# Kernel optimization log

Hardware: AMD Instinct MI355X
Metric: run time of the kernel (lower is better)

Reference implementation:

```python
import jax, jax.numpy as jnp
import numpy as np

NG = 1024      # graphs
NPG = 128      # nodes per graph (forced by lin1 = Linear(128*hid, 128))
N = NG * NPG   # 131072 nodes
DEG = 16       # avg in-graph degree
E = N * DEG    # 2,097,152 edges
IN, H = 4, 64


def setup_inputs() -> dict:
    key = jax.random.key(0)
    ks = jax.random.split(key, 24)
    x = jax.random.normal(ks[0], (N, IN), jnp.float32)
    # edges constrained within each 128-node graph
    src = jax.random.randint(ks[1], (E,), 0, NPG)
    dst = jax.random.randint(ks[2], (E,), 0, NPG)
    off = jnp.repeat(jnp.arange(NG, dtype=jnp.int32) * NPG, NPG * DEG)
    edge_index = jnp.stack([src.astype(jnp.int32) + off, dst.astype(jnp.int32) + off])
    g = lambda k, shp, fan: jax.random.normal(k, shp, jnp.float32) / np.float32(np.sqrt(fan))
    return {
        "x": x, "edge_index": edge_index,
        # GATv2Conv(4->64)
        "Wl": g(ks[3], (IN, H), IN), "bl": jnp.zeros((H,), jnp.float32),
        "Wr": g(ks[4], (IN, H), IN), "br": jnp.zeros((H,), jnp.float32),
        "att_v2": g(ks[5], (H,), H), "b_v2": jnp.zeros((H,), jnp.float32),
        # GATConv #1 (64->64)
        "Wg1": g(ks[6], (H, H), H), "as1": g(ks[7], (H,), H),
        "ad1": g(ks[8], (H,), H), "bg1": jnp.zeros((H,), jnp.float32),
        # GATConv #2 (64->64)
        "Wg2": g(ks[9], (H, H), H), "as2": g(ks[10], (H,), H),
        "ad2": g(ks[11], (H,), H), "bg2": jnp.zeros((H,), jnp.float32),
        # LayerNorm(64)
        "ln_g": jnp.ones((H,), jnp.float32), "ln_b": jnp.zeros((H,), jnp.float32),
        # heads: Linear(128*64 -> 128), Linear(128 -> 1)
        "W1": g(ks[12], (NPG * H, 128), NPG * H), "b1": jnp.zeros((128,), jnp.float32),
        "W2": g(ks[13], (128, 1), 128), "b2": jnp.zeros((1,), jnp.float32),
    }


def _seg_softmax(logits, seg):
    # stable softmax over edges grouped by destination node
    m = jax.ops.segment_max(logits, seg, num_segments=N)
    ex = jnp.exp(logits - m[seg])
    s = jax.ops.segment_sum(ex, seg, num_segments=N)
    return ex / (s[seg] + 1e-16)


def _gatv2(x, src, dst, Wl, bl, Wr, br, att, bias):
    xl = x @ Wl + bl                       # source transform [N,H]
    xr = x @ Wr + br                       # target transform [N,H]
    e = jax.nn.leaky_relu(xl[src] + xr[dst], 0.2) @ att   # [E]
    a = _seg_softmax(e, dst)
    out = jax.ops.segment_sum(a[:, None] * xl[src], dst, num_segments=N)
    return out + bias


def _gat(x, src, dst, W, a_src, a_dst, bias):
    # GATConv default: add self-loops
    loop = jnp.arange(N, dtype=src.dtype)
    s2 = jnp.concatenate([src, loop]); d2 = jnp.concatenate([dst, loop])
    xw = x @ W                             # [N,H]
    al_s = xw @ a_src; al_d = xw @ a_dst   # per-node attention halves [N]
    e = jax.nn.leaky_relu(al_s[s2] + al_d[d2], 0.2)
    a = _seg_softmax(e, d2)
    out = jax.ops.segment_sum(a[:, None] * xw[s2], d2, num_segments=N)
    return out + bias


def _layernorm(x, g, b, eps=1e-5):
    mu = jnp.mean(x, -1, keepdims=True)
    var = jnp.mean(jnp.square(x - mu), -1, keepdims=True)
    return (x - mu) * jax.lax.rsqrt(var + eps) * g + b


def reference(x, edge_index, Wl, bl, Wr, br, att_v2, b_v2,
              Wg1, as1, ad1, bg1, Wg2, as2, ad2, bg2,
              ln_g, ln_b, W1, b1, W2, b2):
    src, dst = edge_index[0], edge_index[1]
    h = jax.nn.leaky_relu(_gatv2(x, src, dst, Wl, bl, Wr, br, att_v2, b_v2), 0.01)
    h = _layernorm(h, ln_g, ln_b)
    h = jax.nn.relu(_gat(h, src, dst, Wg1, as1, ad1, bg1))
    h = jax.nn.relu(_gat(h, src, dst, Wg2, as2, ad2, bg2))
    # linearize: batch is sorted with exactly NPG nodes per graph -> reshape
    h = h.reshape(NG, NPG * H)
    h = jax.nn.leaky_relu(h @ W1 + b1, 0.01)
    return jax.nn.sigmoid(h @ W2 + b2)     # [NG, 1]
```

## Files before the change

### kernel.cpp

```cpp
#include <hip/hip_runtime.h>
#include <hip/hip_bf16.h>
#include <hip/hip_fp16.h>

#define NGRAPH 1024
#define NPG 128
#define EPG 2048
#define ETOT (NGRAPH*NPG*16)

typedef unsigned int uint;
typedef unsigned short ushort_t;
typedef __attribute__((ext_vector_type(2))) _Float16 h2v;
typedef __attribute__((ext_vector_type(8))) _Float16 h8v;
typedef __attribute__((ext_vector_type(4))) float f32x4;

#define MFMA16H __builtin_amdgcn_mfma_f32_16x16x32_f16
#define FDOT2(a,b,c) __builtin_amdgcn_fdot2((a),(b),(c),false)

union U1H2 { uint u; h2v h; };
union U4H8 { uint4 u; h8v h; };
union U4H2 { uint4 u; h2v h[4]; };

__device__ __forceinline__ float lrelu(float x, float s){ return fmaxf(x, x*s); }
__device__ __forceinline__ uint pkh(float a, float b){
  U1H2 t; t.h.x = (_Float16)a; t.h.y = (_Float16)b; return t.u;
}
__device__ __forceinline__ ushort_t hfb(float v){
  union { _Float16 h; ushort_t u; } t; t.h = (_Float16)v; return t.u;
}
__device__ __forceinline__ float2 uph(uint u){
  U1H2 t; t.u = u;
  return float2{(float)t.h.x, (float)t.h.y};
}
#define DPP_ADD(v, ctrl) ((v) + __int_as_float(__builtin_amdgcn_update_dpp(0, __float_as_int(v), (ctrl), 0xF, 0xF, false)))

__device__ __forceinline__ int oswz(int r, int p){ return (r<<5) | ((((p>>2) ^ (r & 7))<<2) | (p & 3)); }
__device__ __forceinline__ int obase(int r, int oc){ return (r<<5) | (((oc) ^ (r & 7))<<2); }

__device__ __forceinline__ void fma8(float* acc, uint4 q, float a){
  float2 f0 = uph(q.x), f1 = uph(q.y), f2 = uph(q.z), f3 = uph(q.w);
  acc[0] += a*f0.x; acc[1] += a*f0.y;
  acc[2] += a*f1.x; acc[3] += a*f1.y;
  acc[4] += a*f2.x; acc[5] += a*f2.y;
  acc[6] += a*f3.x; acc[7] += a*f3.y;
}

__device__ __forceinline__ float dotp(uint ul, uint ur, h2v a2, float acc){
  U1H2 l, r; l.u = ul; r.u = ur;
  h2v v = l.h + r.h;
  U1H2 sv; sv.h = v;
  U1H2 av; av.u = sv.u & 0x7FFF7FFFu;
  h2v c6; c6.x = (_Float16)0.6f; c6.y = (_Float16)0.6f;
  h2v c4; c4.x = (_Float16)0.4f; c4.y = (_Float16)0.4f;
  h2v w = v * c6 + av.h * c4;
  return FDOT2(w, a2, acc);
}

#define O_A   0
#define O_B   4096
#define O_EVA 8192
#define O_ED  10240
#define O_WS  11264
#define O_SOF 11392
#define O_ALS 11457
#define O_ALD 11585
#define SM_SZ 11713

__global__ __launch_bounds__(256, 3) void gnn_fused(
    const float* __restrict__ x, const int* __restrict__ ei,
    const float* __restrict__ Wl, const float* __restrict__ bl,
    const float* __restrict__ Wr, const float* __restrict__ br,
    const float* __restrict__ att, const float* __restrict__ bv2,
    const float* __restrict__ Wg1, const float* __restrict__ as1,
    const float* __restrict__ ad1, const float* __restrict__ bg1,
    const float* __restrict__ Wg2, const float* __restrict__ as2,
    const float* __restrict__ ad2, const float* __restrict__ bg2,
    const float* __restrict__ lng, const float* __restrict__ lnb,
    uint* __restrict__ hout)
{
  __shared__ uint SM[SM_SZ];
  float*    eva    = (float*)(SM + O_EVA);
  ushort_t* edsL   = (ushort_t*)(SM + O_ED);
  ushort_t* soff16 = (ushort_t*)(SM + O_SOF);
  float*    als    = (float*)(SM + O_ALS);
  float*    ald    = (float*)(SM + O_ALD);
  float*    was    = (float*)(SM + O_WS);
  float*    wad    = was + 64;
  ushort_t* wgA16  = (ushort_t*)(SM + O_A);
  ushort_t* wg16   = (ushort_t*)(SM + O_EVA);

  const int g    = blockIdx.x;
  const int tid  = threadIdx.x;
  const int lane = tid & 63;
  const int wv   = tid >> 6;
  const int lw   = lane & 15;
  const int lq   = lane >> 4;
  const int sl   = lane & 7;
  const int grp  = lane >> 3;
  const int ebase = g * EPG;

  {
    int* spos = (int*)(SM + O_EVA);
    if (tid < NPG) spos[tid] = 0;
    __syncthreads();
    for (int e = tid; e < EPG; e += 256)
      atomicAdd(&spos[ei[ETOT + ebase + e] - g*NPG], 1);
    __syncthreads();
    if (wv == 0) {
      int c0 = spos[lane], c1 = spos[lane + 64];
      #pragma unroll
      for (int o = 1; o < 64; o <<= 1) { int t = __shfl_up(c0, o); if (lane >= o) c0 += t; }
      #pragma unroll
      for (int o = 1; o < 64; o <<= 1) { int t = __shfl_up(c1, o); if (lane >= o) c1 += t; }
      int tot0 = __shfl(c0, 63);
      soff16[lane + 1]  = (ushort_t)c0;
      soff16[lane + 65] = (ushort_t)(c1 + tot0);
      if (lane == 0) soff16[0] = 0;
    }
    __syncthreads();
    if (tid < NPG) spos[tid] = soff16[tid];
    __syncthreads();
    for (int e = tid; e < EPG; e += 256) {
      int s = ei[ebase + e] - g*NPG;
      int d = ei[ETOT + ebase + e] - g*NPG;
      int p = atomicAdd(&spos[d], 1);
      edsL[p] = (ushort_t)(s | (d << 8));
    }
  }

  {
    const int pl = lane & 31, hb = lane >> 5;
    const float2 wl0 = *(const float2*)&Wl[0*64 + 2*pl];
    const float2 wl1 = *(const float2*)&Wl[1*64 + 2*pl];
    const float2 wl2 = *(const float2*)&Wl[2*64 + 2*pl];
    const float2 wl3 = *(const float2*)&Wl[3*64 + 2*pl];
    const float2 wr0 = *(const float2*)&Wr[0*64 + 2*pl];
    const float2 wr1 = *(const float2*)&Wr[1*64 + 2*pl];
    const float2 wr2 = *(const float2*)&Wr[2*64 + 2*pl];
    const float2 wr3 = *(const float2*)&Wr[3*64 + 2*pl];
    const float2 blp = *(const float2*)&bl[2*pl];
    const float2 brp = *(const float2*)&br[2*pl];
    const float4* x4 = (const float4*)x + (size_t)g * NPG;
    for (int st = 0; st < 16; st++) {
      int i = st*8 + wv*2 + hb;
      float4 xi = x4[i];
      float l0 = blp.x + xi.x*wl0.x + xi.y*wl1.x + xi.z*wl2.x + xi.w*wl3.x;
      float l1 = blp.y + xi.x*wl0.y + xi.y*wl1.y + xi.z*wl2.y + xi.w*wl3.y;
      float r0 = brp.x + xi.x*wr0.x + xi.y*wr1.x + xi.z*wr2.x + xi.w*wr3.x;
      float r1 = brp.y + xi.x*wr0.y + xi.y*wr1.y + xi.z*wr2.y + xi.w*wr3.y;
      SM[O_A + oswz(i, pl)] = pkh(l0, l1);
      SM[O_B + oswz(i, pl)] = pkh(r0, r1);
    }
  }
  __syncthreads();

  {
    h2v att2[32];
    #pragma unroll
    for (int p2 = 0; p2 < 32; p2++) {
      att2[p2].x = (_Float16)att[2*p2];
      att2[p2].y = (_Float16)att[2*p2 + 1];
    }
    for (int it = 0; it < 8; it++) {
      int e  = tid + it*256;
      int sd = edsL[e];
      int s  = sd & 127, d = sd >> 8;
      float acc = 0.f;
      #pragma unroll
      for (int c = 0; c < 8; c++) {
        uint4 ql = *(uint4*)&SM[O_A + obase(s, c)];
        uint4 qr = *(uint4*)&SM[O_B + obase(d, c)];
        acc = dotp(ql.x, qr.x, att2[4*c+0], acc);
        acc = dotp(ql.y, qr.y, att2[4*c+1], acc);
        acc = dotp(ql.z, qr.z, att2[4*c+2], acc);
        acc = dotp(ql.w, qr.w, att2[4*c+3], acc);
      }
      eva[e] = acc;
    }
  }
  __syncthreads();

  {
    const int dd = tid >> 4, sl16 = tid & 15;
    for (int it = 0; it < 8; it++) {
      int d = it*16 + dd;
      int p0 = soff16[d], p1 = soff16[d+1];
      float m = -1e30f;
      for (int p = p0 + sl16; p < p1; p += 16) m = fmaxf(m, eva[p]);
      #pragma unroll
      for (int o = 1; o < 16; o <<= 1) m = fmaxf(m, __shfl_xor(m, o));
      float ss = 0.f;
      for (int p = p0 + sl16; p < p1; p += 16) {
        float ex = __expf(eva[p] - m); ss += ex; eva[p] = ex;
      }
      #pragma unroll
      for (int o = 1; o < 16; o <<= 1) ss += __shfl_xor(ss, o);
      if (sl16 == 0) als[d] = 1.f / (ss + 1e-16f);
    }
  }
  __syncthreads();

  {
    float2 bvA = *(const float2*)&bv2[sl*8];
    float2 bvB = *(const float2*)&bv2[sl*8 + 2];
    float2 bvC = *(const float2*)&bv2[sl*8 + 4];
    float2 bvD = *(const float2*)&bv2[sl*8 + 6];
    for (int pass = 0; pass < 4; pass++) {
      int d  = wv*32 + pass*8 + grp;
      int p0 = soff16[d], p1 = soff16[d+1];
      float acc[8] = {0,0,0,0,0,0,0,0};
      if (p0 < p1) {
        int sN = edsL[p0] & 127;
        uint4 qN = *(uint4*)&SM[O_A + obase(sN, sl)];
        float wN = eva[p0];
        for (int e = p0; e < p1; e++) {
          uint4 ql = qN; float w = wN;
          if (e + 1 < p1) {
            sN = edsL[e+1] & 127;
            qN = *(uint4*)&SM[O_A + obase(sN, sl)];
            wN = eva[e+1];
          }
          fma8(acc, ql, w);
        }
      }
      float nm = als[d];
      uint4 o;
      o.x = pkh(lrelu(acc[0]*nm+bvA.x,0.01f), lrelu(acc[1]*nm+bvA.y,0.01f));
      o.y = pkh(lrelu(acc[2]*nm+bvB.x,0.01f), lrelu(acc[3]*nm+bvB.y,0.01f));
      o.z = pkh(lrelu(acc[4]*nm+bvC.x,0.01f), lrelu(acc[5]*nm+bvC.y,0.01f));
      o.w = pkh(lrelu(acc[6]*nm+bvD.x,0.01f), lrelu(acc[7]*nm+bvD.y,0.01f));
      *(uint4*)&SM[O_B + obase(d, sl)] = o;
    }
  }
  __syncthreads();

  {
    int pl = lane & 31, hb = lane >> 5;
    float2 gv = *(const float2*)&lng[2*pl];
    float2 bv = *(const float2*)&lnb[2*pl];
    h2v one2; one2.x = (_Float16)1.f; one2.y = (_Float16)1.f;
    for (int it = 0; it < 16; it++) {
      int d = it*8 + wv*2 + hb;
      uint w = SM[O_B + oswz(d, pl)];
      U1H2 t; t.u = w;
      float s1 = FDOT2(t.h, one2, 0.f);
      float s2 = FDOT2(t.h, t.h, 0.f);
      #pragma unroll
      for (int o = 1; o < 32; o <<= 1) { s1 += __shfl_xor(s1, o); s2 += __shfl_xor(s2, o); }
      float mu  = s1 * 0.015625f;
      float var = s2 * 0.015625f - mu*mu;
      float rs  = rsqrtf(var + 1e-5f);
      float2 f = uph(w);
      SM[O_B + oswz(d, pl)] = pkh((f.x-mu)*rs*gv.x + bv.x, (f.y-mu)*rs*gv.y + bv.y);
    }
  }
  __syncthreads();

  for (int layer = 0; layer < 2; layer++) {
    const float* Wg  = layer ? Wg2 : Wg1;
    const float* avs = layer ? as2 : as1;
    const float* avd = layer ? ad2 : ad1;
    const float* bg  = layer ? bg2 : bg1;

    if (tid < 128) {
      const float* av = (tid < 64) ? avs : avd;
      float* dst = (tid < 64) ? was : wad;
      int k = tid & 63;
      float acc = 0.f;
      #pragma unroll
      for (int jj = 0; jj < 16; jj++) {
        float4 w = *(const float4*)&Wg[k*64 + jj*4];
        float4 a = *(const float4*)&av[jj*4];
        acc += w.x*a.x + w.y*a.y + w.z*a.z + w.w*a.w;
      }
      dst[k] = acc;
    } else {
      int t2 = tid - 128;
      #pragma unroll
      for (int i = 0; i < 8; i++) {
        int idx = t2 + i*128;
        int k = idx >> 4, j4 = (idx & 15)*4;
        float4 w = *(const float4*)&Wg[k*64 + j4];
        wg16[oswz(j4+0, k>>1)*2 + (k&1)] = hfb(w.x);
        wg16[oswz(j4+1, k>>1)*2 + (k&1)] = hfb(w.y);
        wg16[oswz(j4+2, k>>1)*2 + (k&1)] = hfb(w.z);
        wg16[oswz(j4+3, k>>1)*2 + (k&1)] = hfb(w.w);
      }
    }
    __syncthreads();

    {
      U4H8 a0t, a1t;
      a0t.u = *(uint4*)&SM[O_EVA + obase(16*wv + lw, lq)];
      a1t.u = *(uint4*)&SM[O_EVA + obase(16*wv + lw, 4+lq)];
      int j0 = 16*wv + lq*4;
      #pragma unroll
      for (int nt = 0; nt < 8; nt++) {
        int d = nt*16 + lw;
        U4H8 b0t, b1t;
        b0t.u = *(uint4*)&SM[O_B + obase(d, lq)];
        b1t.u = *(uint4*)&SM[O_B + obase(d, 4+lq)];
        f32x4 c = {0.f,0.f,0.f,0.f};
        c = MFMA16H(a0t.h, b0t.h, c, 0, 0, 0);
        c = MFMA16H(a1t.h, b1t.h, c, 0, 0, 0);
        #pragma unroll
        for (int rg = 0; rg < 4; rg++) {
          int j = j0 + rg;
          wgA16[oswz(d, j>>1)*2 + (j&1)] = hfb(c[rg]);
        }
      }
      h2v ws2[4], wd2[4];
      #pragma unroll
      for (int q2 = 0; q2 < 4; q2++) {
        float2 a = *(float2*)&was[sl*8 + 2*q2];
        float2 b = *(float2*)&wad[sl*8 + 2*q2];
        ws2[q2].x = (_Float16)a.x; ws2[q2].y = (_Float16)a.y;
        wd2[q2].x = (_Float16)b.x; wd2[q2].y = (_Float16)b.y;
      }
      for (int ps = 0; ps < 4; ps++) {
        int n = ps*32 + (tid >> 3);
        U4H2 q; q.u = *(uint4*)&SM[O_B + obase(n, sl)];
        float sa = 0.f, sd = 0.f;
        #pragma unroll
        for (int q2 = 0; q2 < 4; q2++) {
          sa = FDOT2(q.h[q2], ws2[q2], sa);
          sd = FDOT2(q.h[q2], wd2[q2], sd);
        }
        sa = DPP_ADD(sa, 0x111); sa = DPP_ADD(sa, 0x112); sa = DPP_ADD(sa, 0x114);
        sd = DPP_ADD(sd, 0x111); sd = DPP_ADD(sd, 0x112); sd = DPP_ADD(sd, 0x114);
        if ((lane & 7) == 7) { als[n] = sa; ald[n] = sd; }
      }
    }
    __syncthreads();

    for (int it = 0; it < 8; it++) {
      int e  = tid + it*256;
      int sd = edsL[e];
      eva[e] = lrelu(als[sd & 127] + ald[sd >> 8], 0.2f);
    }
    __syncthreads();

    {
      const int dd = tid >> 4, sl16 = tid & 15;
      for (int it = 0; it < 8; it++) {
        int d = it*16 + dd;
        int p0 = soff16[d], p1 = soff16[d+1];
        float lgs = lrelu(als[d] + ald[d], 0.2f);
        float m = lgs;
        for (int p = p0 + sl16; p < p1; p += 16) m = fmaxf(m, eva[p]);
        #pragma unroll
        for (int o = 1; o < 16; o <<= 1) m = fmaxf(m, __shfl_xor(m, o));
        float ex0 = __expf(lgs - m);
        float ss = 0.f;
        for (int p = p0 + sl16; p < p1; p += 16) {
          float ex = __expf(eva[p] - m); ss += ex; eva[p] = ex;
        }
        #pragma unroll
        for (int o = 1; o < 16; o <<= 1) ss += __shfl_xor(ss, o);
        if (sl16 == 0) {
          als[d] = ex0;
          ald[d] = 1.f / (ss + ex0 + 1e-16f);
        }
      }
    }
    __syncthreads();

    {
      float2 bgA = *(const float2*)&bg[sl*8];
      float2 bgB = *(const float2*)&bg[sl*8 + 2];
      float2 bgC = *(const float2*)&bg[sl*8 + 4];
      float2 bgD = *(const float2*)&bg[sl*8 + 6];
      for (int pass = 0; pass < 4; pass++) {
        int d  = wv*32 + pass*8 + grp;
        int p0 = soff16[d], p1 = soff16[d+1];
        float acc[8] = {0,0,0,0,0,0,0,0};
        fma8(acc, *(uint4*)&SM[O_A + obase(d, sl)], als[d]);
        if (p0 < p1) {
          int sN = edsL[p0] & 127;
          uint4 qN = *(uint4*)&SM[O_A + obase(sN, sl)];
          float wN = eva[p0];
          for (int e = p0; e < p1; e++) {
            uint4 ql = qN; float w = wN;
            if (e + 1 < p1) {
              sN = edsL[e+1] & 127;
              qN = *(uint4*)&SM[O_A + obase(sN, sl)];
              wN = eva[e+1];
            }
            fma8(acc, ql, w);
          }
        }
        float nm = ald[d];
        uint4 o;
        o.x = pkh(fmaxf(acc[0]*nm+bgA.x,0.f), fmaxf(acc[1]*nm+bgA.y,0.f));
        o.y = pkh(fmaxf(acc[2]*nm+bgB.x,0.f), fmaxf(acc[3]*nm+bgB.y,0.f));
        o.z = pkh(fmaxf(acc[4]*nm+bgC.x,0.f), fmaxf(acc[5]*nm+bgC.y,0.f));
        o.w = pkh(fmaxf(acc[6]*nm+bgD.x,0.f), fmaxf(acc[7]*nm+bgD.y,0.f));
        *(uint4*)&SM[O_B + obase(d, sl)] = o;
      }
    }
    __syncthreads();
  }

  {
    uint* hg = hout + (size_t)g * 4096;
    #pragma unroll
    for (int i = 0; i < 16; i++) {
      int idx = tid + i*256;
      hg[idx] = SM[O_B + oswz(idx >> 5, idx & 31)];
    }
  }
}

__global__ __launch_bounds__(256) void head_gemm(
    const uint* __restrict__ hbuf, const float* __restrict__ W1,
    float* __restrict__ partial)
{
  __shared__ uint sAh[2048];
  __shared__ uint sBh[4096];
  const int tid = threadIdx.x, lane = tid & 63, wv = tid >> 6;
  const int lw = lane & 15, lq = lane >> 4;
  const int g0 = blockIdx.x * 64;
  const int ks = blockIdx.y;
  f32x4 acc[8];
  #pragma unroll
  for (int i = 0; i < 8; i++) acc[i] = f32x4{0.f,0.f,0.f,0.f};

  for (int ch = 0; ch < 8; ch++) {
    int pb  = ks*256 + ch*32;
    int kk0 = ks*512 + ch*64;
    #pragma unroll
    for (int i = 0; i < 2; i++) {
      int idx = tid + i*256; int r = idx >> 3, q4 = idx & 7;
      uint4 v = *(const uint4*)&hbuf[(size_t)(g0+r)*4096 + pb + q4*4];
      *(uint4*)&sAh[(r<<5) | ((q4 ^ (r & 7))<<2)] = v;
    }
    #pragma unroll
    for (int i = 0; i < 16; i++) {
      int idx = tid + i*256;
      int c = idx & 127, kp = idx >> 7;
      int kk = kk0 + 2*kp;
      sBh[oswz(c, kp)] = pkh(W1[(size_t)kk*128 + c], W1[(size_t)(kk+1)*128 + c]);
    }
    __syncthreads();
    U4H8 a0t, a1t;
    a0t.u = *(uint4*)&sAh[obase(16*wv + lw, lq)];
    a1t.u = *(uint4*)&sAh[obase(16*wv + lw, 4+lq)];
    #pragma unroll
    for (int nt = 0; nt < 8; nt++) {
      int c = nt*16 + lw;
      U4H8 b0t, b1t;
      b0t.u = *(uint4*)&sBh[obase(c, lq)];
      b1t.u = *(uint4*)&sBh[obase(c, 4+lq)];
      acc[nt] = MFMA16H(a0t.h, b0t.h, acc[nt], 0, 0, 0);
      acc[nt] = MFMA16H(a1t.h, b1t.h, acc[nt], 0, 0, 0);
    }
    __syncthreads();
  }
  float* pp = partial + (size_t)ks*131072;
  #pragma unroll
  for (int nt = 0; nt < 8; nt++) {
    int c = nt*16 + lw;
    int r0 = g0 + 16*wv + lq*4;
    #pragma unroll
    for (int rg = 0; rg < 4; rg++)
      pp[(size_t)(r0+rg)*128 + c] = acc[nt][rg];
  }
}

__global__ __launch_bounds__(256) void head_out(
    const float* __restrict__ partial, const float* __restrict__ b1,
    const float* __restrict__ W2, const float* __restrict__ b2,
    float* __restrict__ out)
{
  const int tid = threadIdx.x;
  const int gl  = tid >> 5;
  const int c4  = tid & 31;
  const int g   = blockIdx.x*8 + gl;
  float4 v = *(const float4*)&b1[c4*4];
  #pragma unroll
  for (int s = 0; s < 16; s++) {
    float4 p = *(const float4*)&partial[(size_t)s*131072 + (size_t)g*128 + c4*4];
    v.x += p.x; v.y += p.y; v.z += p.z; v.w += p.w;
  }
  float4 w = *(const float4*)&W2[c4*4];
  float t = lrelu(v.x,0.01f)*w.x + lrelu(v.y,0.01f)*w.y
          + lrelu(v.z,0.01f)*w.z + lrelu(v.w,0.01f)*w.w;
  #pragma unroll
  for (int m = 1; m < 32; m <<= 1) t += __shfl_xor(t, m);
  if (c4 == 0) out[g] = 1.f / (1.f + __expf(-(t + b2[0])));
}

extern "C" void kernel_launch(void* const* d_in, const int* in_sizes, int n_in,
                              void* d_out, int out_size, void* d_ws, size_t ws_size,
                              hipStream_t stream) {
  const float* x   = (const float*)d_in[0];
  const int*   ei  = (const int*)  d_in[1];
  const float* Wl  = (const float*)d_in[2];
  const float* bl_ = (const float*)d_in[3];
  const float* Wr  = (const float*)d_in[4];
  const float* br_ = (const float*)d_in[5];
  const float* att = (const float*)d_in[6];
  const float* bv2 = (const float*)d_in[7];
  const float* Wg1 = (const float*)d_in[8];
  const float* as1 = (const float*)d_in[9];
  const float* ad1 = (const float*)d_in[10];
  const float* bg1 = (const float*)d_in[11];
  const float* Wg2 = (const float*)d_in[12];
  const float* as2 = (const float*)d_in[13];
  const float* ad2 = (const float*)d_in[14];
  const float* bg2 = (const float*)d_in[15];
  const float* lng = (const float*)d_in[16];
  const float* lnb = (const float*)d_in[17];
  const float* W1  = (const float*)d_in[18];
  const float* b1  = (const float*)d_in[19];
  const float* W2  = (const float*)d_in[20];
  const float* b2  = (const float*)d_in[21];
  float* out = (float*)d_out;

  uint*  hbuf    = (uint*)d_ws;
  float* partial = (float*)((char*)d_ws + (size_t)16*1024*1024);

  gnn_fused<<<NGRAPH, 256, 0, stream>>>(x, ei, Wl, bl_, Wr, br_, att, bv2,
      Wg1, as1, ad1, bg1, Wg2, as2, ad2, bg2, lng, lnb, hbuf);
  head_gemm<<<dim3(16, 16), 256, 0, stream>>>(hbuf, W1, partial);
  head_out<<<128, 256, 0, stream>>>(partial, b1, W2, b2, out);
}
```

Baseline: 310.2 us.

## Factor GATv2 logits into per-node terms, fp16 aggregation, deeper head split-K

```diff
diff --git a/kernel.cpp b/kernel.cpp
--- a/kernel.cpp
+++ b/kernel.cpp
@@ -42,17 +42,6 @@
   acc[2] += a*f1.x; acc[3] += a*f1.y;
   acc[4] += a*f2.x; acc[5] += a*f2.y;
   acc[6] += a*f3.x; acc[7] += a*f3.y;
-}
-
-__device__ __forceinline__ float dotp(uint ul, uint ur, h2v a2, float acc){
-  U1H2 l, r; l.u = ul; r.u = ur;
-  h2v v = l.h + r.h;
-  U1H2 sv; sv.h = v;
-  U1H2 av; av.u = sv.u & 0x7FFF7FFFu;
-  h2v c6; c6.x = (_Float16)0.6f; c6.y = (_Float16)0.6f;
-  h2v c4; c4.x = (_Float16)0.4f; c4.y = (_Float16)0.4f;
-  h2v w = v * c6 + av.h * c4;
-  return FDOT2(w, a2, acc);
 }
 
 #define O_A   0
@@ -153,28 +142,46 @@
   }
   __syncthreads();
 
-  {
-    h2v att2[32];
+  h2v a06[4], a04[4];
+  #pragma unroll
+  for (int q2 = 0; q2 < 4; q2++) {
+    float2 a = *(const float2*)&att[sl*8 + 2*q2];
+    a06[q2].x = (_Float16)(0.6f*a.x); a06[q2].y = (_Float16)(0.6f*a.y);
+    a04[q2].x = (_Float16)(0.4f*a.x); a04[q2].y = (_Float16)(0.4f*a.y);
+  }
+
+  for (int ps = 0; ps < 4; ps++) {
+    int n = ps*32 + (tid >> 3);
+    U4H2 ql; ql.u = *(uint4*)&SM[O_A + obase(n, sl)];
+    U4H2 qr; qr.u = *(uint4*)&SM[O_B + obase(n, sl)];
+    float su = 0.f, sw = 0.f;
     #pragma unroll
-    for (int p2 = 0; p2 < 32; p2++) {
-      att2[p2].x = (_Float16)att[2*p2];
-      att2[p2].y = (_Float16)att[2*p2 + 1];
-    }
-    for (int it = 0; it < 8; it++) {
-      int e  = tid + it*256;
+    for (int q2 = 0; q2 < 4; q2++) {
+      su = FDOT2(ql.h[q2], a06[q2], su);
+      sw = FDOT2(qr.h[q2], a06[q2], sw);
+    }
+    su = DPP_ADD(su, 0x111); su = DPP_ADD(su, 0x112); su = DPP_ADD(su, 0x114);
+    sw = DPP_ADD(sw, 0x111); sw = DPP_ADD(sw, 0x112); sw = DPP_ADD(sw, 0x114);
+    if ((lane & 7) == 7) { als[n] = su; ald[n] = sw; }
+  }
+  __syncthreads();
+
+  {
+    for (int step = 0; step < 64; step++) {
+      int e  = wv*512 + step*8 + grp;
       int sd = edsL[e];
       int s  = sd & 127, d = sd >> 8;
+      U4H2 ql; ql.u = *(uint4*)&SM[O_A + obase(s, sl)];
+      U4H2 qr; qr.u = *(uint4*)&SM[O_B + obase(d, sl)];
       float acc = 0.f;
       #pragma unroll
-      for (int c = 0; c < 8; c++) {
-        uint4 ql = *(uint4*)&SM[O_A + obase(s, c)];
-        uint4 qr = *(uint4*)&SM[O_B + obase(d, c)];
-        acc = dotp(ql.x, qr.x, att2[4*c+0], acc);
-        acc = dotp(ql.y, qr.y, att2[4*c+1], acc);
-        acc = dotp(ql.z, qr.z, att2[4*c+2], acc);
-        acc = dotp(ql.w, qr.w, att2[4*c+3], acc);
-      }
-      eva[e] = acc;
+      for (int q2 = 0; q2 < 4; q2++) {
+        h2v v = ql.h[q2] + qr.h[q2];
+        U1H2 t; t.h = v; t.u &= 0x7FFF7FFFu;
+        acc = FDOT2(t.h, a04[q2], acc);
+      }
+      acc = DPP_ADD(acc, 0x111); acc = DPP_ADD(acc, 0x112); acc = DPP_ADD(acc, 0x114);
+      if (sl == 7) eva[e] = acc + als[s] + ald[d];
     }
   }
   __syncthreads();
@@ -372,28 +379,36 @@
       for (int pass = 0; pass < 4; pass++) {
         int d  = wv*32 + pass*8 + grp;
         int p0 = soff16[d], p1 = soff16[d+1];
-        float acc[8] = {0,0,0,0,0,0,0,0};
-        fma8(acc, *(uint4*)&SM[O_A + obase(d, sl)], als[d]);
+        _Float16 hw0 = (_Float16)als[d];
+        h2v w2; w2.x = hw0; w2.y = hw0;
+        U4H2 acc2, qs;
+        qs.u = *(uint4*)&SM[O_A + obase(d, sl)];
+        #pragma unroll
+        for (int q2 = 0; q2 < 4; q2++) acc2.h[q2] = qs.h[q2] * w2;
         if (p0 < p1) {
           int sN = edsL[p0] & 127;
           uint4 qN = *(uint4*)&SM[O_A + obase(sN, sl)];
           float wN = eva[p0];
           for (int e = p0; e < p1; e++) {
-            uint4 ql = qN; float w = wN;
+            U4H2 ql; ql.u = qN; float w = wN;
             if (e + 1 < p1) {
               sN = edsL[e+1] & 127;
               qN = *(uint4*)&SM[O_A + obase(sN, sl)];
               wN = eva[e+1];
             }
-            fma8(acc, ql, w);
+            _Float16 hw = (_Float16)w;
+            h2v we2; we2.x = hw; we2.y = hw;
+            #pragma unroll
+            for (int q2 = 0; q2 < 4; q2++) acc2.h[q2] += ql.h[q2] * we2;
           }
         }
         float nm = ald[d];
+        float2 r0 = uph(acc2.u.x), r1 = uph(acc2.u.y), r2 = uph(acc2.u.z), r3 = uph(acc2.u.w);
         uint4 o;
-        o.x = pkh(fmaxf(acc[0]*nm+bgA.x,0.f), fmaxf(acc[1]*nm+bgA.y,0.f));
-        o.y = pkh(fmaxf(acc[2]*nm+bgB.x,0.f), fmaxf(acc[3]*nm+bgB.y,0.f));
-        o.z = pkh(fmaxf(acc[4]*nm+bgC.x,0.f), fmaxf(acc[5]*nm+bgC.y,0.f));
-        o.w = pkh(fmaxf(acc[6]*nm+bgD.x,0.f), fmaxf(acc[7]*nm+bgD.y,0.f));
+        o.x = pkh(fmaxf(r0.x*nm+bgA.x,0.f), fmaxf(r0.y*nm+bgA.y,0.f));
+        o.y = pkh(fmaxf(r1.x*nm+bgB.x,0.f), fmaxf(r1.y*nm+bgB.y,0.f));
+        o.z = pkh(fmaxf(r2.x*nm+bgC.x,0.f), fmaxf(r2.y*nm+bgC.y,0.f));
+        o.w = pkh(fmaxf(r3.x*nm+bgD.x,0.f), fmaxf(r3.y*nm+bgD.y,0.f));
         *(uint4*)&SM[O_B + obase(d, sl)] = o;
       }
     }
@@ -424,9 +439,9 @@
   #pragma unroll
   for (int i = 0; i < 8; i++) acc[i] = f32x4{0.f,0.f,0.f,0.f};
 
-  for (int ch = 0; ch < 8; ch++) {
-    int pb  = ks*256 + ch*32;
-    int kk0 = ks*512 + ch*64;
+  for (int ch = 0; ch < 4; ch++) {
+    int pb  = ks*128 + ch*32;
+    int kk0 = ks*256 + ch*64;
     #pragma unroll
     for (int i = 0; i < 2; i++) {
       int idx = tid + i*256; int r = idx >> 3, q4 = idx & 7;
@@ -477,7 +492,7 @@
   const int g   = blockIdx.x*8 + gl;
   float4 v = *(const float4*)&b1[c4*4];
   #pragma unroll
-  for (int s = 0; s < 16; s++) {
+  for (int s = 0; s < 32; s++) {
     float4 p = *(const float4*)&partial[(size_t)s*131072 + (size_t)g*128 + c4*4];
     v.x += p.x; v.y += p.y; v.z += p.z; v.w += p.w;
   }
@@ -521,6 +536,6 @@
 
   gnn_fused<<<NGRAPH, 256, 0, stream>>>(x, ei, Wl, bl_, Wr, br_, att, bv2,
       Wg1, as1, ad1, bg1, Wg2, as2, ad2, bg2, lng, lnb, hbuf);
-  head_gemm<<<dim3(16, 16), 256, 0, stream>>>(hbuf, W1, partial);
+  head_gemm<<<dim3(16, 32), 256, 0, stream>>>(hbuf, W1, partial);
   head_out<<<128, 256, 0, stream>>>(partial, b1, W2, b2, out);
 }
```

After: 301.6 us. 2.8% less time.
